# Optimization experiments

Measured on AMD Instinct MI355X. Metric: run time of the kernel, lower is better.

The kernel has to match this reference:

```python
import jax, jax.numpy as jnp
import numpy as np
from jax import lax

B, N, G, K, D = 16, 8192, 512, 32, 128
MLP = [128, 128, 256]
EPS = 1e-5


def setup_inputs() -> dict:
    key = jax.random.key(0)
    ks = jax.random.split(key, 2 + len(MLP))
    inp = {
        "xyz": jax.random.normal(ks[0], (B, N, 3), jnp.float32),
        "points": jax.random.normal(ks[1], (B, N, D), jnp.float32),
    }
    last = D
    for li, oc in enumerate(MLP, 1):
        inp[f"W{li}"] = jax.random.normal(ks[1 + li], (oc, last), jnp.float32) / np.float32(np.sqrt(last))
        inp[f"b{li}"] = jnp.zeros((oc,), jnp.float32)
        inp[f"g{li}"] = jnp.ones((oc,), jnp.float32)
        inp[f"be{li}"] = jnp.zeros((oc,), jnp.float32)
        last = oc
    return inp


def _fps(xyz, num_group):
    # farthest point sampling, deterministic start at index 0 -> idx [B, G]
    b, n, _ = xyz.shape
    init_idx = jnp.zeros((b,), jnp.int32)

    def step(carry, _):
        dists, last_idx = carry                                   # [B,N], [B]
        last = jnp.take_along_axis(xyz, last_idx[:, None, None], axis=1)  # [B,1,3]
        d = jnp.sum((xyz - last) ** 2, axis=-1)                   # [B,N]
        dists = jnp.minimum(dists, d)
        nxt = jnp.argmax(dists, axis=1).astype(jnp.int32)
        return (dists, nxt), nxt

    init = (jnp.full((b, n), 1e10, jnp.float32), init_idx)
    _, rest = lax.scan(step, init, None, length=num_group - 1)    # [G-1, B]
    return jnp.concatenate([init_idx[None, :], rest], axis=0).T   # [B, G]


def _forward(xyz, points, layers):
    b = xyz.shape[0]
    center_idx = _fps(xyz, G)                                       # [B,G]
    center = jnp.take_along_axis(xyz, center_idx[:, :, None], axis=1)  # [B,G,3]
    # KNN: pairwise squared distances center->points, top-k smallest
    d2 = (jnp.sum(center ** 2, -1)[:, :, None]
          + jnp.sum(xyz ** 2, -1)[:, None, :]
          - 2.0 * jnp.einsum("bgc,bnc->bgn", center, xyz))          # [B,G,N]
    _, idx = lax.top_k(-d2, K)                                      # [B,G,K]
    feats = jnp.take_along_axis(points, idx.reshape(b, G * K, 1), axis=1)
    feats = feats.reshape(b, G, K, -1)                              # [B,G,K,D]
    x = feats.transpose(0, 3, 2, 1)                                 # [B,D,K,G]
    for (W, bb, g, be) in layers:
        x = jnp.einsum("oc,bckg->bokg", W, x) + bb[None, :, None, None]
        m = jnp.mean(x, axis=(0, 2, 3), keepdims=True)
        v = jnp.var(x, axis=(0, 2, 3), keepdims=True)               # biased, as torch BN
        x = (x - m) * lax.rsqrt(v + EPS) * g[None, :, None, None] + be[None, :, None, None]
        x = jax.nn.relu(x)
    new_points = jnp.max(x, axis=2).transpose(0, 2, 1)              # [B,G,C_out]
    return center, new_points


def reference(xyz, points, W1, b1, g1, be1, W2, b2, g2, be2, W3, b3, g3, be3):
    layers = [(W1, b1, g1, be1), (W2, b2, g2, be2), (W3, b3, g3, be3)]
    return _forward(xyz, points, layers)
```

## Files before the change

### kernel.cpp

```cpp
#include <hip/hip_runtime.h>
#include <hip/hip_bf16.h>

#define BB 16
#define NN 8192
#define GG 512
#define KK 32
#define DD 128

typedef __attribute__((ext_vector_type(8))) short bf16x8;
typedef __attribute__((ext_vector_type(4))) float f32x4;
typedef __attribute__((ext_vector_type(2))) float f32x2;
typedef __attribute__((ext_vector_type(2))) unsigned int u32x2;
typedef __attribute__((ext_vector_type(4))) unsigned int u32x4;
typedef __attribute__((ext_vector_type(2))) unsigned long long u64x2;

__device__ __forceinline__ unsigned short f2bf(float f){
  unsigned int u = __builtin_bit_cast(unsigned int, f);
  unsigned int r = (u + 0x7FFFu + ((u >> 16) & 1u)) >> 16;
  return (unsigned short)r;
}
__device__ __forceinline__ float bf2f(unsigned short h){
  unsigned int u = ((unsigned int)h) << 16;
  return __builtin_bit_cast(float, u);
}

__device__ __forceinline__ float wave_max_f32(float v){
  int x = __builtin_bit_cast(int, v);
#define STEPMAX(C) { int y = __builtin_amdgcn_update_dpp(x, x, C, 0xF, 0xF, false); \
  float f = fmaxf(__builtin_bit_cast(float,x), __builtin_bit_cast(float,y)); x = __builtin_bit_cast(int,f); }
  STEPMAX(0x111) STEPMAX(0x112) STEPMAX(0x114) STEPMAX(0x118) STEPMAX(0x142) STEPMAX(0x143)
#undef STEPMAX
  return __builtin_bit_cast(float, __builtin_amdgcn_readlane(x, 63));
}
__device__ __forceinline__ float wave_min_f32(float v){
  int x = __builtin_bit_cast(int, v);
#define STEPMIN(C) { int y = __builtin_amdgcn_update_dpp(x, x, C, 0xF, 0xF, false); \
  float f = fminf(__builtin_bit_cast(float,x), __builtin_bit_cast(float,y)); x = __builtin_bit_cast(int,f); }
  STEPMIN(0x111) STEPMIN(0x112) STEPMIN(0x114) STEPMIN(0x118) STEPMIN(0x142) STEPMIN(0x143)
#undef STEPMIN
  return __builtin_bit_cast(float, __builtin_amdgcn_readlane(x, 63));
}
__device__ __forceinline__ int wave_min_i32(int v){
  int x = v;
#define STEPMNI(C) { int y = __builtin_amdgcn_update_dpp(x, x, C, 0xF, 0xF, false); \
  x = (y < x) ? y : x; }
  STEPMNI(0x111) STEPMNI(0x112) STEPMNI(0x114) STEPMNI(0x118) STEPMNI(0x142) STEPMNI(0x143)
#undef STEPMNI
  return __builtin_amdgcn_readlane(x, 63);
}

__device__ __forceinline__ void knn_group(int bg, int t128,
    const float* __restrict__ xs, const float* __restrict__ ys,
    const float* __restrict__ zs, const float* __restrict__ pps,
    const float* __restrict__ center, int* __restrict__ kidx,
    unsigned long long (*wlist)[KK], int* outidx)
{
#pragma clang fp contract(off)
  int lane = t128 & 63, w = t128 >> 6;
  int b = bg >> 9;
  const float cx = center[(size_t)bg*3+0];
  const float cy = center[(size_t)bg*3+1];
  const float cz = center[(size_t)bg*3+2];
  const float ccv = (cx*cx + cy*cy) + cz*cz;
  const float* xb = xs  + (size_t)b*NN;
  const float* yb = ys  + (size_t)b*NN;
  const float* zb = zs  + (size_t)b*NN;
  const float* pb = pps + (size_t)b*NN;

  f32x2 d2v[32];
  float gmin[8]; int gidx[8];
#pragma unroll
  for (int gi = 0; gi < 8; ++gi){ gmin[gi] = 3.4e38f; gidx[gi] = 0x7FFFFFFF; }
  int nb = w*128 + 2*lane;
  f32x2 cxv = (f32x2){cx, cx}, cyv = (f32x2){cy, cy}, czv = (f32x2){cz, cz};
  f32x2 ccvv = (f32x2){ccv, ccv};
#pragma unroll
  for (int q = 0; q < 32; ++q){
    int n0 = q*256 + nb;
    f32x2 x = *(const f32x2*)(xb + n0);
    f32x2 y = *(const f32x2*)(yb + n0);
    f32x2 z = *(const f32x2*)(zb + n0);
    f32x2 pp = *(const f32x2*)(pb + n0);
    f32x2 dot = (cxv*x + cyv*y) + czv*z;
    f32x2 d = (ccvv + pp) - 2.0f*dot;
    d2v[q] = d;
    int gi = q >> 2;
    if (d.x < gmin[gi]){ gmin[gi] = d.x; gidx[gi] = n0; }
    if (d.y < gmin[gi]){ gmin[gi] = d.y; gidx[gi] = n0 + 1; }
  }
  float bv = gmin[0]; int bi = gidx[0];
#pragma unroll
  for (int gi = 1; gi < 8; ++gi)
    if (gmin[gi] < bv){ bv = gmin[gi]; bi = gidx[gi]; }

  unsigned long long mykey = ~0ULL;
  for (int k = 0; k < KK; ++k){
    float wmin = wave_min_f32(bv);
    unsigned long long mask = __ballot(bv == wmin);
    int n_win;
    if (__popcll(mask) == 1){
      n_win = __builtin_amdgcn_readlane(bi, (int)__builtin_ctzll(mask));
    } else {
      int cand = (bv == wmin) ? bi : 0x7FFFFFFF;
      n_win = wave_min_i32(cand);
    }
    if (lane == k){
      unsigned int fm = __builtin_bit_cast(unsigned int, wmin);
      unsigned int mapd = fm ^ (unsigned int)(((int)fm >> 31) | 0x80000000);
      mykey = ((unsigned long long)mapd << 32) | (unsigned int)n_win;
    }
    if (bi == n_win){
#define RESCAN2(GI) { \
      float nm = 3.4e38f; int ni = 0x7FFFFFFF; \
      _Pragma("unroll") \
      for (int j = 0; j < 4; ++j){ \
        int q = GI*4 + j; \
        int n0 = q*256 + nb; \
        f32x2 v = d2v[q]; \
        if (n0 == n_win) v.x = 3.4e38f; \
        if (n0 + 1 == n_win) v.y = 3.4e38f; \
        d2v[q] = v; \
        if (v.x < nm){ nm = v.x; ni = n0; } \
        if (v.y < nm){ nm = v.y; ni = n0 + 1; } } \
      gmin[GI] = nm; gidx[GI] = ni; }
      switch (n_win >> 10){
        case 0: RESCAN2(0); break;
        case 1: RESCAN2(1); break;
        case 2: RESCAN2(2); break;
        case 3: RESCAN2(3); break;
        case 4: RESCAN2(4); break;
        case 5: RESCAN2(5); break;
        case 6: RESCAN2(6); break;
        default: RESCAN2(7); break;
      }
#undef RESCAN2
      bv = gmin[0]; bi = gidx[0];
#pragma unroll
      for (int gi = 1; gi < 8; ++gi)
        if (gmin[gi] < bv){ bv = gmin[gi]; bi = gidx[gi]; }
    }
  }

  if (lane < KK) wlist[w][lane] = mykey;
  __syncthreads();
  if (lane < KK){
    unsigned long long K = mykey;
    const unsigned long long* other = wlist[1 - w];
    int cnt = 0;
#pragma unroll
    for (int j = 0; j < KK; ++j) cnt += (other[j] < K) ? 1 : 0;
    int rank = lane + cnt;
    if (rank < KK) outidx[rank] = (int)(unsigned int)K;
  }
  __syncthreads();
  if (t128 < KK) kidx[(size_t)bg*KK + t128] = outidx[t128];
}

__device__ __forceinline__ void fps_part(const float* __restrict__ xyz,
    float* __restrict__ center_out, float* __restrict__ ddws,
    int b, int t, int g0, int g1, bool save_dd, char* lds)
{
#pragma clang fp contract(off)
  float (*tbl)[4]    = (float(*)[4])lds;
  float (*outbuf)[4] = (float(*)[4])(lds + 131072);
  unsigned long long (*slot)[2] =
      (unsigned long long(*)[2])(lds + 131072 + 2048);
  int lane = t & 63, wid = t >> 6;
  const float* base = xyz + (size_t)b * NN * 3;
  f32x2 px[4], py[4], pz[4], dd[4];
  if (g0 == 1){
#pragma unroll
    for (int i = 0; i < 4; ++i) dd[i] = (f32x2){1e10f, 1e10f};
  } else {
    const float* dp = ddws + ((size_t)b*1024 + t)*8;
    f32x4 s0 = *(const f32x4*)dp;
    f32x4 s1 = *(const f32x4*)(dp + 4);
    dd[0] = (f32x2){s0[0], s0[1]};
    dd[1] = (f32x2){s0[2], s0[3]};
    dd[2] = (f32x2){s1[0], s1[1]};
    dd[3] = (f32x2){s1[2], s1[3]};
  }
#pragma unroll
  for (int i = 0; i < 4; ++i){
    int n0 = i*2048 + t, n1 = n0 + 1024;
    float x0 = base[n0*3+0], y0 = base[n0*3+1], z0 = base[n0*3+2];
    float x1 = base[n1*3+0], y1 = base[n1*3+1], z1 = base[n1*3+2];
    px[i] = (f32x2){x0, x1}; py[i] = (f32x2){y0, y1}; pz[i] = (f32x2){z0, z1};
    f32x4 c0 = {x0, y0, z0, 0.f}, c1 = {x1, y1, z1, 0.f};
    *(f32x4*)&tbl[n0][0] = c0;
    *(f32x4*)&tbl[n1][0] = c1;
  }
  float lx, ly, lz;
  if (g0 == 1){ lx = base[0]; ly = base[1]; lz = base[2]; }
  else {
    lx = center_out[((size_t)b*GG + g0 - 1)*3 + 0];
    ly = center_out[((size_t)b*GG + g0 - 1)*3 + 1];
    lz = center_out[((size_t)b*GG + g0 - 1)*3 + 2];
  }
  if (t < 6) slot[t >> 1][t & 1] = 0;
  __syncthreads();
  for (int g = g0; g < g1; ++g){
    f32x2 lxv = (f32x2){lx, lx}, lyv = (f32x2){ly, ly}, lzv = (f32x2){lz, lz};
    f32x2 vm = (f32x2){-1.f, -1.f};
#pragma unroll
    for (int i = 0; i < 4; ++i){
      f32x2 dx = px[i] - lxv, dy = py[i] - lyv, dz = pz[i] - lzv;
      f32x2 s = (dx*dx + dy*dy) + dz*dz;
      f32x2 nd = __builtin_elementwise_min(dd[i], s);
      dd[i] = nd;
      vm = __builtin_elementwise_max(vm, nd);
    }
    float m = fmaxf(vm.x, vm.y);
    int mi = 0x7FFFFFFF;
#pragma unroll
    for (int i = 3; i >= 0; --i){
      int n0 = i*2048 + t;
      if (dd[i].y == m) mi = n0 + 1024;
      if (dd[i].x == m) mi = n0;
    }
    float wmax = wave_max_f32(m);
    bool cnd = (m == wmax);
    unsigned long long mask = __ballot(cnd);
    int n_wave;
    if (__popcll(mask) == 1){
      n_wave = __builtin_amdgcn_readlane(mi, (int)__builtin_ctzll(mask));
    } else {
      int cand = cnd ? mi : 0x7FFFFFFF;
      n_wave = wave_min_i32(cand);
    }
    unsigned long long key =
        ((unsigned long long)__builtin_bit_cast(unsigned int, wmax) << 32)
      | (unsigned int)(~n_wave);
    int p = g - (g/3)*3;
    if (lane == 0) atomicMax(&slot[p][wid & 1], key);
    __syncthreads();
    u64x2 sA = *(const u64x2*)&slot[p][0];
    unsigned long long M = sA.x > sA.y ? sA.x : sA.y;
    int n_win = (int)~((unsigned int)M);
    f32x4 cw = *(const f32x4*)&tbl[n_win][0];
    lx = cw[0]; ly = cw[1]; lz = cw[2];
    if (t == 0) *(f32x4*)&outbuf[g - g0][0] = cw;
    if (t < 2){
      int z = p + 2; if (z >= 3) z -= 3;
      slot[z][t] = 0;
    }
  }
  __syncthreads();
  if (t < g1 - g0){
    int g = g0 + t;
    center_out[((size_t)b*GG + g)*3 + 0] = outbuf[t][0];
    center_out[((size_t)b*GG + g)*3 + 1] = outbuf[t][1];
    center_out[((size_t)b*GG + g)*3 + 2] = outbuf[t][2];
  }
  if (g0 == 1 && t == 0){
    center_out[((size_t)b*GG)*3 + 0] = base[0];
    center_out[((size_t)b*GG)*3 + 1] = base[1];
    center_out[((size_t)b*GG)*3 + 2] = base[2];
  }
  if (save_dd){
    f32x4 s0 = {dd[0].x, dd[0].y, dd[1].x, dd[1].y};
    f32x4 s1 = {dd[2].x, dd[2].y, dd[3].x, dd[3].y};
    float* dp = ddws + ((size_t)b*1024 + t)*8;
    *(f32x4*)dp       = s0;
    *(f32x4*)(dp + 4) = s1;
  }
}

template<int OC, int MODE, bool STATS, bool STORE, bool POOL>
__device__ __forceinline__ void gemm_body(int sbid, int t,
    const unsigned short* __restrict__ Wbf, const float* __restrict__ bias,
    const unsigned short* __restrict__ pointsbf, const int* __restrict__ kidx,
    const unsigned short* __restrict__ Xin,
    const float* __restrict__ psum_in, const float* __restrict__ gin,
    const float* __restrict__ bein,
    unsigned short* __restrict__ Yout, float* __restrict__ psum,
    float* __restrict__ rawmax, float* __restrict__ rawmin,
    unsigned short* smem, float* ssc, float* ssh)
{
  constexpr int MF = OC / 64;
  int l = t & 63, w = t >> 6;
  int l15 = l & 15, lh = l >> 4;
  int jbase = sbid * 64;
  int obase = w * (OC / 4);
  int slot = sbid & 63;

  if constexpr (MODE == 1){
    if (t < 128){
      float s = 0.f, q = 0.f;
#pragma unroll
      for (int sl = 0; sl < 64; ++sl){
        s += psum_in[sl*128 + t];
        q += psum_in[64*128 + sl*128 + t];
      }
      const float inv = 1.f / 262144.f;
      float mean = s * inv;
      float var  = q * inv - mean*mean;
      float sc = gin[t] * rsqrtf(var + 1e-5f);
      ssc[t] = sc;
      ssh[t] = bein[t] - mean*sc;
    }
  }

  bf16x8 a[MF][4];
#pragma unroll
  for (int m = 0; m < MF; ++m)
#pragma unroll
    for (int kf = 0; kf < 4; ++kf){
      int row = obase + m*16 + l15;
      int c8  = kf*32 + lh*8;
      a[m][kf] = *(const bf16x8*)(Wbf + (size_t)row*128 + c8);
    }

  if constexpr (MODE == 1) __syncthreads();

#pragma unroll
  for (int q = 0; q < 4; ++q){
    int ci = q*256 + t;
    int j = ci >> 4, cc = ci & 15;
    unsigned short* dst = &smem[j*128 + ((cc ^ (j & 15)) * 8)];
    if constexpr (MODE == 0){
      int jg = jbase + j;
      int bb = jg >> 14;
      int row = kidx[jg];
      const unsigned short* src = pointsbf + ((size_t)bb*NN + row)*DD + cc*8;
      *(u32x4*)dst = *(const u32x4*)src;
    } else {
      const unsigned short* src = Xin + ((size_t)(jbase + j))*128 + cc*8;
      u32x4 v = *(const u32x4*)src;
      int c0 = cc * 8;
      unsigned int wo[4];
#pragma unroll
      for (int p = 0; p < 4; ++p){
        float x0 = bf2f((unsigned short)(v[p] & 0xFFFFu));
        float x1 = bf2f((unsigned short)(v[p] >> 16));
        x0 = fmaxf(fmaf(x0, ssc[c0 + 2*p],     ssh[c0 + 2*p]),     0.f);
        x1 = fmaxf(fmaf(x1, ssc[c0 + 2*p + 1], ssh[c0 + 2*p + 1]), 0.f);
        wo[p] = f2bf(x0) | ((unsigned int)f2bf(x1) << 16);
      }
      u32x4 pv = {wo[0], wo[1], wo[2], wo[3]};
      *(u32x4*)dst = pv;
    }
  }
  __syncthreads();

  f32x4 acc[MF][4];
#pragma unroll
  for (int m = 0; m < MF; ++m)
#pragma unroll
    for (int n = 0; n < 4; ++n)
      acc[m][n] = (f32x4){0.f, 0.f, 0.f, 0.f};

#pragma unroll
  for (int n = 0; n < 4; ++n){
    bf16x8 bfr[4];
    int j = n*16 + l15;
#pragma unroll
    for (int kf = 0; kf < 4; ++kf){
      int ch = kf*4 + lh;
      bfr[kf] = *(const bf16x8*)&smem[j*128 + ((ch ^ (j & 15)) * 8)];
    }
#pragma unroll
    for (int m = 0; m < MF; ++m)
#pragma unroll
      for (int kf = 0; kf < 4; ++kf)
        acc[m][n] = __builtin_amdgcn_mfma_f32_16x16x32_bf16(a[m][kf], bfr[kf], acc[m][n], 0, 0, 0);
  }

#pragma unroll
  for (int m = 0; m < MF; ++m){
    int o0 = obase + m*16 + lh*4;
    f32x4 bv = *(const f32x4*)(bias + o0);
#pragma unroll
    for (int n = 0; n < 4; ++n) acc[m][n] += bv;
  }

  if constexpr (STATS){
#pragma unroll
    for (int m = 0; m < MF; ++m){
#pragma unroll
      for (int r = 0; r < 4; ++r){
        float s = 0.f, q2 = 0.f;
#pragma unroll
        for (int n = 0; n < 4; ++n){ float v = acc[m][n][r]; s += v; q2 += v*v; }
        s  += __shfl_xor(s, 1);  s  += __shfl_xor(s, 2);  s  += __shfl_xor(s, 4);  s  += __shfl_xor(s, 8);
        q2 += __shfl_xor(q2, 1); q2 += __shfl_xor(q2, 2); q2 += __shfl_xor(q2, 4); q2 += __shfl_xor(q2, 8);
        if (l15 == 0){
          int o = obase + m*16 + lh*4 + r;
          atomicAdd(psum + slot*OC + o, s);
          atomicAdd(psum + 64*OC + slot*OC + o, q2);
        }
      }
    }
  }

  if constexpr (POOL){
#pragma unroll
    for (int m = 0; m < MF; ++m){
      int o0 = obase + m*16 + lh*4;
      f32x4 gmx0, gmx1, gmn0, gmn1;
#pragma unroll
      for (int r = 0; r < 4; ++r){
        float v0 = acc[m][0][r], v1 = acc[m][1][r];
        float v2 = acc[m][2][r], v3 = acc[m][3][r];
        float ax0 = fmaxf(v0, v1), ax1 = fmaxf(v2, v3);
        float an0 = fminf(v0, v1), an1 = fminf(v2, v3);
#pragma unroll
        for (int mk = 1; mk < 16; mk <<= 1){
          ax0 = fmaxf(ax0, __shfl_xor(ax0, mk));
          ax1 = fmaxf(ax1, __shfl_xor(ax1, mk));
          an0 = fminf(an0, __shfl_xor(an0, mk));
          an1 = fminf(an1, __shfl_xor(an1, mk));
        }
        gmx0[r] = ax0; gmx1[r] = ax1; gmn0[r] = an0; gmn1[r] = an1;
      }
      if (l15 == 0){
        int gg = jbase >> 5;
        *(f32x4*)(rawmax + (size_t)gg*256 + o0)       = gmx0;
        *(f32x4*)(rawmax + (size_t)(gg + 1)*256 + o0) = gmx1;
        *(f32x4*)(rawmin + (size_t)gg*256 + o0)       = gmn0;
        *(f32x4*)(rawmin + (size_t)(gg + 1)*256 + o0) = gmn1;
      }
    }
  }

  if constexpr (STORE){
    __syncthreads();
#pragma unroll
    for (int m = 0; m < MF; ++m){
      int o0 = obase + m*16 + lh*4;
      int co = o0 >> 2;
#pragma unroll
      for (int n = 0; n < 4; ++n){
        int j = n*16 + l15;
        unsigned int w0 = f2bf(acc[m][n][0]) | ((unsigned int)f2bf(acc[m][n][1]) << 16);
        unsigned int w1 = f2bf(acc[m][n][2]) | ((unsigned int)f2bf(acc[m][n][3]) << 16);
        u32x2 pv = {w0, w1};
        *(u32x2*)&smem[j*OC + ((co ^ ((j & 15) << 1)) * 4)] = pv;
      }
    }
    __syncthreads();
    constexpr int CPR = OC / 4;
    constexpr int CPT = (64 * CPR) / 256;
#pragma unroll
    for (int q = 0; q < CPT; ++q){
      int ci = q*256 + t;
      int j = ci / CPR, co = ci % CPR;
      u32x2 v = *(const u32x2*)&smem[j*OC + ((co ^ ((j & 15) << 1)) * 4)];
      *(u32x2*)(Yout + (size_t)(jbase + j)*OC + co*4) = v;
    }
  }
}

#define LDSB (131072 + 2048 + 64)

template<int PH>
__global__ __launch_bounds__(1024)
void fps_phase(const float* __restrict__ xyz, const float* __restrict__ points,
               const float* __restrict__ W1, const float* __restrict__ W2,
               const float* __restrict__ W3,
               float* __restrict__ center_out, float* __restrict__ ddws,
               float* __restrict__ xs, float* __restrict__ ys,
               float* __restrict__ zs, float* __restrict__ pps,
               unsigned short* __restrict__ Wbf,
               unsigned short* __restrict__ pointsbf,
               int* __restrict__ kidx,
               const float* __restrict__ b1,
               unsigned short* __restrict__ Y1, float* __restrict__ psumA)
{
  __shared__ __attribute__((aligned(16))) char lds[LDSB];
  int t = threadIdx.x;
  if (blockIdx.x < BB){
    constexpr int g0 = (PH == 0) ? 1 : PH*128;
    constexpr int g1 = (PH + 1)*128;
    fps_part(xyz, center_out, ddws, blockIdx.x, t, g0, g1, PH < 3, lds);
    return;
  }
  if constexpr (PH == 0){
#pragma clang fp contract(off)
    int pb = blockIdx.x - BB;
    size_t i = ((size_t)pb*1024 + t)*8;
    f32x4 u0 = *(const f32x4*)(points + i);
    f32x4 u1 = *(const f32x4*)(points + i + 4);
    unsigned int w0 = f2bf(u0[0]) | ((unsigned int)f2bf(u0[1]) << 16);
    unsigned int w1 = f2bf(u0[2]) | ((unsigned int)f2bf(u0[3]) << 16);
    unsigned int w2 = f2bf(u1[0]) | ((unsigned int)f2bf(u1[1]) << 16);
    unsigned int w3 = f2bf(u1[2]) | ((unsigned int)f2bf(u1[3]) << 16);
    u32x4 pv = {w0, w1, w2, w3};
    *(u32x4*)(pointsbf + i) = pv;
    if (pb < 128){
      int n = pb*1024 + t;
      float x = xyz[(size_t)n*3 + 0];
      float y = xyz[(size_t)n*3 + 1];
      float z = xyz[(size_t)n*3 + 2];
      xs[n] = x; ys[n] = y; zs[n] = z;
      pps[n] = (x*x + y*y) + z*z;
    }
    if (pb < 64){
      int n = pb*1024 + t;
      float v;
      if (n < 16384)      v = W1[n];
      else if (n < 32768) v = W2[n - 16384];
      else                v = W3[n - 32768];
      Wbf[n] = f2bf(v);
    }
  } else {
    int pb = blockIdx.x - BB;
    if (pb < 256){
      unsigned long long (*kwl)[2][KK] = (unsigned long long(*)[2][KK])lds;
      int* kout = (int*)(lds + 8*2*KK*8);
      int sub = t >> 7, t128 = t & 127;
      int idx = pb*8 + sub;
      int b = idx >> 7, g = (PH-1)*128 + (idx & 127);
      knn_group(b*GG + g, t128, xs, ys, zs, pps, center_out, kidx,
                &kwl[sub][0], kout + sub*KK);
    } else if constexpr (PH >= 2){
      int hb = pb - 256;
      int sub = t >> 8, t256 = t & 255;
      int u = hb*4 + sub;
      int us = (u & 7) * 128 + (u >> 3);
      int b = us >> 6, tau = (PH-2)*64 + (us & 63);
      int sbid = b*256 + tau;
      unsigned short* smem = (unsigned short*)(lds + sub*16384);
      gemm_body<128, 0, true, true, false>(sbid, t256,
          Wbf, b1, pointsbf, kidx, nullptr, nullptr, nullptr, nullptr,
          Y1, psumA, nullptr, nullptr, smem, nullptr, nullptr);
    }
  }
}

__global__ __launch_bounds__(256)
void knn_gemm_tail(const float* __restrict__ xs, const float* __restrict__ ys,
                   const float* __restrict__ zs, const float* __restrict__ pps,
                   const float* __restrict__ center, int* __restrict__ kidx,
                   const unsigned short* __restrict__ Wbf,
                   const float* __restrict__ b1,
                   const unsigned short* __restrict__ pointsbf,
                   unsigned short* __restrict__ Y1, float* __restrict__ psumA)
{
  __shared__ unsigned short smem[64 * 128];
  __shared__ unsigned long long kwl[2][2][KK] __attribute__((aligned(16)));
  __shared__ int kout[2][KK];
  int bid = blockIdx.x, t = threadIdx.x;
  if (bid < 1024){
    int swz = (bid & 7) * 128 + (bid >> 3);
    int sub = t >> 7, t128 = t & 127;
    int idx = swz*2 + sub;
    int b = idx >> 7, g = 384 + (idx & 127);
    knn_group(b*GG + g, t128, xs, ys, zs, pps, center, kidx,
              kwl[sub], kout[sub]);
    return;
  }
  int h = bid - 1024;
  int hs = (h & 7) * 128 + (h >> 3);
  int b = hs >> 6, tau = 128 + (hs & 63);
  gemm_body<128, 0, true, true, false>(b*256 + tau, t,
      Wbf, b1, pointsbf, kidx, nullptr, nullptr, nullptr, nullptr,
      Y1, psumA, nullptr, nullptr, smem, nullptr, nullptr);
}

__global__ __launch_bounds__(256)
void gemm1d_kernel(const unsigned short* __restrict__ Wbf, const float* __restrict__ b1,
                   const unsigned short* __restrict__ pointsbf,
                   const int* __restrict__ kidx,
                   unsigned short* __restrict__ Y1, float* __restrict__ psumA)
{
  __shared__ unsigned short smem[64 * 128];
  int bid = blockIdx.x, t = threadIdx.x;
  int hs = (bid & 7) * 128 + (bid >> 3);
  int b = hs >> 6, tau = 192 + (hs & 63);
  gemm_body<128, 0, true, true, false>(b*256 + tau, t,
      Wbf, b1, pointsbf, kidx, nullptr, nullptr, nullptr, nullptr,
      Y1, psumA, nullptr, nullptr, smem, nullptr, nullptr);
}

template<int OC, int MODE, bool STATS, bool STORE, bool POOL>
__global__ __launch_bounds__(256)
void gemm_kernel(const unsigned short* __restrict__ Wbf, const float* __restrict__ bias,
                 const unsigned short* __restrict__ Xin,
                 const float* __restrict__ psum_in, const float* __restrict__ gin,
                 const float* __restrict__ bein,
                 unsigned short* __restrict__ Yout, float* __restrict__ psum,
                 float* __restrict__ rawmax, float* __restrict__ rawmin)
{
  __shared__ unsigned short smem[64 * OC];
  __shared__ float ssc[128], ssh[128];
  int bid = blockIdx.x, t = threadIdx.x;
  int sbid = (bid & 7) * 512 + (bid >> 3);
  gemm_body<OC, MODE, STATS, STORE, POOL>(sbid, t,
      Wbf, bias, nullptr, nullptr, Xin, psum_in, gin, bein,
      Yout, psum, rawmax, rawmin, smem, ssc, ssh);
}

__global__ __launch_bounds__(256)
void finish3_kernel(const float* __restrict__ psumC, const float* __restrict__ g3,
                    const float* __restrict__ be3, const float* __restrict__ rawmax,
                    const float* __restrict__ rawmin, float* __restrict__ opool)
{
  __shared__ float ssc[256], ssh[256];
  int t = threadIdx.x;
  {
    float s = 0.f, q = 0.f;
#pragma unroll
    for (int sl = 0; sl < 64; ++sl){
      s += psumC[sl*256 + t];
      q += psumC[64*256 + sl*256 + t];
    }
    const float inv = 1.f / 262144.f;
    float mean = s * inv;
    float var  = q * inv - mean*mean;
    float sc = g3[t] * rsqrtf(var + 1e-5f);
    ssc[t] = sc;
    ssh[t] = be3[t] - mean*sc;
  }
  __syncthreads();
  float sc = ssc[t], sh = ssh[t];
  int gg0 = blockIdx.x * 16;
#pragma unroll
  for (int i = 0; i < 16; ++i){
    int gg = gg0 + i;
    float rv = (sc >= 0.f) ? rawmax[(size_t)gg*256 + t] : rawmin[(size_t)gg*256 + t];
    opool[(size_t)gg*256 + t] = fmaxf(fmaf(rv, sc, sh), 0.f);
  }
}

extern "C" void kernel_launch(void* const* d_in, const int* in_sizes, int n_in,
                              void* d_out, int out_size, void* d_ws, size_t ws_size,
                              hipStream_t stream)
{
  const float* xyz    = (const float*)d_in[0];
  const float* points = (const float*)d_in[1];
  const float* W1  = (const float*)d_in[2];
  const float* b1  = (const float*)d_in[3];
  const float* g1  = (const float*)d_in[4];
  const float* be1 = (const float*)d_in[5];
  const float* W2  = (const float*)d_in[6];
  const float* b2  = (const float*)d_in[7];
  const float* g2  = (const float*)d_in[8];
  const float* be2 = (const float*)d_in[9];
  const float* W3  = (const float*)d_in[10];
  const float* b3  = (const float*)d_in[11];
  const float* g3  = (const float*)d_in[12];
  const float* be3 = (const float*)d_in[13];

  float* out    = (float*)d_out;
  float* center = out;
  float* opool  = out + (size_t)BB*GG*3;

  char* ws = (char*)d_ws;
  size_t off = 0;
  auto alloc = [&](size_t bytes) -> void* {
    void* p = ws + off;
    off += (bytes + 255) & ~(size_t)255;
    return p;
  };
  unsigned short* Y1   = (unsigned short*)alloc((size_t)262144*128*2);
  unsigned short* Y2   = (unsigned short*)alloc((size_t)262144*128*2);
  int*   kidx = (int*)  alloc((size_t)262144*4);
  unsigned short* Wbf = (unsigned short*)alloc((size_t)65536*2);
  float* rawmax = (float*)alloc((size_t)8192*256*4);
  float* rawmin = (float*)alloc((size_t)8192*256*4);
  float* psumA = (float*)alloc((size_t)2*64*128*4);
  float* psumB = (float*)alloc((size_t)2*64*128*4);
  float* psumC = (float*)alloc((size_t)2*64*256*4);
  float* xsb  = (float*)alloc((size_t)131072*4);
  float* ysb  = (float*)alloc((size_t)131072*4);
  float* zsb  = (float*)alloc((size_t)131072*4);
  float* ppsb = (float*)alloc((size_t)131072*4);
  float* ddws = (float*)alloc((size_t)16*1024*8*4);
  unsigned short* pointsbf = Y2;

  hipMemsetAsync(psumA, 0, (size_t)(2*64*128 + 2*64*128 + 2*64*256)*4 + 1024, stream);

  fps_phase<0><<<BB + 2048, 1024, 0, stream>>>(
      xyz, points, W1, W2, W3, center, ddws, xsb, ysb, zsb, ppsb,
      Wbf, pointsbf, kidx, b1, Y1, psumA);
  fps_phase<1><<<BB + 256, 1024, 0, stream>>>(
      xyz, points, W1, W2, W3, center, ddws, xsb, ysb, zsb, ppsb,
      Wbf, pointsbf, kidx, b1, Y1, psumA);
  fps_phase<2><<<BB + 256 + 256, 1024, 0, stream>>>(
      xyz, points, W1, W2, W3, center, ddws, xsb, ysb, zsb, ppsb,
      Wbf, pointsbf, kidx, b1, Y1, psumA);
  fps_phase<3><<<BB + 256 + 256, 1024, 0, stream>>>(
      xyz, points, W1, W2, W3, center, ddws, xsb, ysb, zsb, ppsb,
      Wbf, pointsbf, kidx, b1, Y1, psumA);

  knn_gemm_tail<<<2048, 256, 0, stream>>>(
      xsb, ysb, zsb, ppsb, center, kidx, Wbf, b1, pointsbf, Y1, psumA);
  gemm1d_kernel<<<1024, 256, 0, stream>>>(Wbf, b1, pointsbf, kidx, Y1, psumA);

  gemm_kernel<128, 1, true, true, false><<<4096, 256, 0, stream>>>(
      Wbf + 16384, b2, Y1, psumA, g1, be1, Y2, psumB, nullptr, nullptr);

  gemm_kernel<256, 1, true, false, true><<<4096, 256, 0, stream>>>(
      Wbf + 32768, b3, Y2, psumB, g2, be2, nullptr, psumC, rawmax, rawmin);

  finish3_kernel<<<512, 256, 0, stream>>>(psumC, g3, be3, rawmax, rawmin, opool);
}
```

Measured before the change: 725.4 us.

## Compute KNN per group in a single wave with register-resident distances

Replaces the two-wave-per-group KNN in the tail kernel with a one-wave-per-group routine. Each lane keeps its 128 distances in registers along with 8 per-bucket minima. The wave then runs 32 rounds of wave-wide argmin, and after each round only the winning lane rescans the bucket that held the winner. This drops the LDS merge and the block barriers, halves the number of KNN blocks, and puts four groups in each block. The cost is heavy register pressure (128 floats per lane), which can spill or lower occupancy, plus 32 serial wave reductions per group.

```diff
diff --git a/kernel.cpp b/kernel.cpp
--- a/kernel.cpp
+++ b/kernel.cpp
@@ -156,6 +156,94 @@
   if (t128 < KK) kidx[(size_t)bg*KK + t128] = outidx[t128];
 }
 
+__device__ __forceinline__ void knn_group1(int bg, int lane,
+    const float* __restrict__ xs, const float* __restrict__ ys,
+    const float* __restrict__ zs, const float* __restrict__ pps,
+    const float* __restrict__ center, int* __restrict__ kidx)
+{
+#pragma clang fp contract(off)
+  int b = bg >> 9;
+  const float cx = center[(size_t)bg*3+0];
+  const float cy = center[(size_t)bg*3+1];
+  const float cz = center[(size_t)bg*3+2];
+  const float ccv = (cx*cx + cy*cy) + cz*cz;
+  const float* xb = xs  + (size_t)b*NN;
+  const float* yb = ys  + (size_t)b*NN;
+  const float* zb = zs  + (size_t)b*NN;
+  const float* pb = pps + (size_t)b*NN;
+
+  f32x2 d2v[64];
+  float gmin[8]; int gidx[8];
+#pragma unroll
+  for (int gi = 0; gi < 8; ++gi){ gmin[gi] = 3.4e38f; gidx[gi] = 0x7FFFFFFF; }
+  int nb = 2*lane;
+  f32x2 cxv = (f32x2){cx, cx}, cyv = (f32x2){cy, cy}, czv = (f32x2){cz, cz};
+  f32x2 ccvv = (f32x2){ccv, ccv};
+#pragma unroll
+  for (int q = 0; q < 64; ++q){
+    int n0 = q*128 + nb;
+    f32x2 x = *(const f32x2*)(xb + n0);
+    f32x2 y = *(const f32x2*)(yb + n0);
+    f32x2 z = *(const f32x2*)(zb + n0);
+    f32x2 pp = *(const f32x2*)(pb + n0);
+    f32x2 dot = (cxv*x + cyv*y) + czv*z;
+    f32x2 d = (ccvv + pp) - 2.0f*dot;
+    d2v[q] = d;
+    int gi = q >> 3;
+    if (d.x < gmin[gi]){ gmin[gi] = d.x; gidx[gi] = n0; }
+    if (d.y < gmin[gi]){ gmin[gi] = d.y; gidx[gi] = n0 + 1; }
+  }
+  float bv = gmin[0]; int bi = gidx[0];
+#pragma unroll
+  for (int gi = 1; gi < 8; ++gi)
+    if (gmin[gi] < bv){ bv = gmin[gi]; bi = gidx[gi]; }
+
+  int kq = 0;
+  for (int k = 0; k < KK; ++k){
+    float wmin = wave_min_f32(bv);
+    unsigned long long mask = __ballot(bv == wmin);
+    int n_win;
+    if (__popcll(mask) == 1){
+      n_win = __builtin_amdgcn_readlane(bi, (int)__builtin_ctzll(mask));
+    } else {
+      int cand = (bv == wmin) ? bi : 0x7FFFFFFF;
+      n_win = wave_min_i32(cand);
+    }
+    if (lane == k) kq = n_win;
+    if (bi == n_win){
+#define RESCAN1(GI) { \
+      float nm = 3.4e38f; int ni = 0x7FFFFFFF; \
+      _Pragma("unroll") \
+      for (int j = 0; j < 8; ++j){ \
+        int q = GI*8 + j; \
+        int n0 = q*128 + nb; \
+        f32x2 v = d2v[q]; \
+        if (n0 == n_win) v.x = 3.4e38f; \
+        if (n0 + 1 == n_win) v.y = 3.4e38f; \
+        d2v[q] = v; \
+        if (v.x < nm){ nm = v.x; ni = n0; } \
+        if (v.y < nm){ nm = v.y; ni = n0 + 1; } } \
+      gmin[GI] = nm; gidx[GI] = ni; }
+      switch (n_win >> 10){
+        case 0: RESCAN1(0); break;
+        case 1: RESCAN1(1); break;
+        case 2: RESCAN1(2); break;
+        case 3: RESCAN1(3); break;
+        case 4: RESCAN1(4); break;
+        case 5: RESCAN1(5); break;
+        case 6: RESCAN1(6); break;
+        default: RESCAN1(7); break;
+      }
+#undef RESCAN1
+      bv = gmin[0]; bi = gidx[0];
+#pragma unroll
+      for (int gi = 1; gi < 8; ++gi)
+        if (gmin[gi] < bv){ bv = gmin[gi]; bi = gidx[gi]; }
+    }
+  }
+  if (lane < KK) kidx[(size_t)bg*KK + lane] = kq;
+}
+
 __device__ __forceinline__ void fps_part(const float* __restrict__ xyz,
     float* __restrict__ center_out, float* __restrict__ ddws,
     int b, int t, int g0, int g1, bool save_dd, char* lds)
@@ -538,19 +626,16 @@
                    unsigned short* __restrict__ Y1, float* __restrict__ psumA)
 {
   __shared__ unsigned short smem[64 * 128];
-  __shared__ unsigned long long kwl[2][2][KK] __attribute__((aligned(16)));
-  __shared__ int kout[2][KK];
   int bid = blockIdx.x, t = threadIdx.x;
-  if (bid < 1024){
-    int swz = (bid & 7) * 128 + (bid >> 3);
-    int sub = t >> 7, t128 = t & 127;
-    int idx = swz*2 + sub;
+  if (bid < 512){
+    int swz = (bid & 7) * 64 + (bid >> 3);
+    int sub = t >> 6, lane = t & 63;
+    int idx = swz*4 + sub;
     int b = idx >> 7, g = 384 + (idx & 127);
-    knn_group(b*GG + g, t128, xs, ys, zs, pps, center, kidx,
-              kwl[sub], kout[sub]);
+    knn_group1(b*GG + g, lane, xs, ys, zs, pps, center, kidx);
     return;
   }
-  int h = bid - 1024;
+  int h = bid - 512;
   int hs = (h & 7) * 128 + (h >> 3);
   int b = hs >> 6, tau = 128 + (hs & 63);
   gemm_body<128, 0, true, true, false>(b*256 + tau, t,
@@ -684,7 +769,7 @@
       xyz, points, W1, W2, W3, center, ddws, xsb, ysb, zsb, ppsb,
       Wbf, pointsbf, kidx, b1, Y1, psumA);
 
-  knn_gemm_tail<<<2048, 256, 0, stream>>>(
+  knn_gemm_tail<<<1536, 256, 0, stream>>>(
       xsb, ysb, zsb, ppsb, center, kidx, Wbf, b1, pointsbf, Y1, psumA);
   gemm1d_kernel<<<1024, 256, 0, stream>>>(Wbf, b1, pointsbf, kidx, Y1, psumA);
 
```

Measured after the change: 753.3 us. 3.9% more time.
